# Kernel optimization log

Measured on AMD Instinct MI355X. Metric: run time of the kernel, lower is better.

Reference implementation:

```python
import jax, jax.numpy as jnp
import numpy as np

B, G = 256, 24
N = B * G
D_IN, HEADS, D_HEAD = 128, 8, 64  # out_channels = in_channels//2 = 64, concat=False
EFF = HEADS * D_HEAD
EPS = 1e-5
SCALE = float(np.sqrt(D_HEAD))

def _gelu(x):
    return jax.nn.gelu(x, approximate=False)

def _pff(x, w1, b1, w2, b2):
    # PositionwiseFeedForward, dropout=0 (eval)
    return _gelu(x @ w1.T + b1) @ w2.T + b2

def _graph_norm_global(x, w, b, ms):
    # GraphNorm called without batch -> single graph over all N nodes
    mean = jnp.mean(x, axis=0, keepdims=True)
    out = x - mean * ms
    var = jnp.mean(out * out, axis=0, keepdims=True)
    return w * out / jnp.sqrt(var + EPS) + b

def _graph_norm(x, w, b, ms, batch, nseg):
    cnt = jax.ops.segment_sum(jnp.ones((x.shape[0],), x.dtype), batch, nseg)[:, None]
    mean = jax.ops.segment_sum(x, batch, nseg) / cnt
    out = x - mean[batch] * ms
    var = jax.ops.segment_sum(out * out, batch, nseg) / cnt
    return w * out / jnp.sqrt(var + EPS)[batch] + b

def _segment_softmax(logits, seg, nseg):
    m = jax.ops.segment_max(logits, seg, num_segments=nseg)
    e = jnp.exp(logits - m[seg])
    s = jax.ops.segment_sum(e, seg, num_segments=nseg)
    return e / (s[seg] + 1e-16)

def _attn_conv(x, edge_index, p):
    (nq_w, nq_b, nq_ms, wq, bq, wk, bk, wv, bv,
     no_w, no_b, no_ms, o_w1, o_b1, o_w2, o_b2) = p
    n = x.shape[0]
    xin = x
    xn = _graph_norm_global(x, nq_w, nq_b, nq_ms)
    q = (xn @ wq.T + bq).reshape(n, HEADS, D_HEAD)
    k = (xn @ wk.T + bk).reshape(n, HEADS, D_HEAD)
    v = (xn @ wv.T + bv).reshape(n, HEADS, D_HEAD)
    loops = jnp.arange(n, dtype=edge_index.dtype)  # add_self_loops appends
    src = jnp.concatenate([edge_index[0], loops])
    dst = jnp.concatenate([edge_index[1], loops])
    qk = jnp.sum(q[dst] * k[src], axis=-1) / SCALE          # [E', H]
    alpha = _segment_softmax(qk, dst, n)                     # segment softmax over dst
    aggr = jax.ops.segment_sum(v[src] * alpha[:, :, None], dst, num_segments=n)  # [N,H,Dh]
    aggr = aggr.mean(axis=1)                                 # concat=False: head mean -> [N,64]
    init = xin.reshape(n, D_IN // D_HEAD, D_HEAD).sum(axis=1)  # sum-fold 128 -> 64 residual
    h = aggr + init
    hn = _graph_norm_global(h, no_w, no_b, no_ms)
    return h + _pff(hn, o_w1, o_b1, o_w2, o_b2)


def setup_inputs() -> dict:
    key = jax.random.key(0)
    ks = jax.random.split(key, 12)
    # block-dense edges: fully connected within each set, no self loops
    a = np.arange(G)
    ii, jj = np.meshgrid(a, a, indexing='ij')
    m = ii != jj
    dst_l, src_l = ii[m], jj[m]
    offs = (np.arange(B) * G)[:, None]
    src = (src_l[None, :] + offs).reshape(-1)
    dst = (dst_l[None, :] + offs).reshape(-1)
    edge_index = jnp.asarray(np.stack([src, dst]), dtype=jnp.int64)
    batch = jnp.asarray(np.repeat(np.arange(B), G), dtype=jnp.int64)
    ptr = jnp.asarray(np.arange(B + 1) * G, dtype=jnp.int64)
    x = jax.random.normal(ks[0], (N, D_IN), jnp.float32)
    def lin(k, o, i):
        return jax.random.normal(k, (o, i), jnp.float32) * (1.0 / np.sqrt(i))
    d = dict(x=x, edge_index=edge_index, ptr=ptr, batch=batch)
    d.update(nq_w=jnp.ones((D_IN,)), nq_b=jnp.zeros((D_IN,)), nq_ms=jnp.ones((D_IN,)))
    d.update(wq=lin(ks[1], EFF, D_IN), bq=jnp.zeros((EFF,)),
             wk=lin(ks[2], EFF, D_IN), bk=jnp.zeros((EFF,)),
             wv=lin(ks[3], EFF, D_IN), bv=jnp.zeros((EFF,)))
    d.update(no_w=jnp.ones((D_HEAD,)), no_b=jnp.zeros((D_HEAD,)), no_ms=jnp.ones((D_HEAD,)))
    d.update(o_w1=lin(ks[4], D_HEAD, D_HEAD), o_b1=jnp.zeros((D_HEAD,)),
             o_w2=lin(ks[5], D_HEAD, D_HEAD), o_b2=jnp.zeros((D_HEAD,)))
    d.update(pn_w=jnp.ones((D_HEAD,)), pn_b=jnp.zeros((D_HEAD,)), pn_ms=jnp.ones((D_HEAD,)))
    d.update(p_w1=lin(ks[6], D_HEAD, D_HEAD), p_b1=jnp.zeros((D_HEAD,)),
             p_w2=lin(ks[7], 1, D_HEAD), p_b2=jnp.zeros((1,)))
    return d


def reference(x, edge_index, ptr, batch,
              nq_w, nq_b, nq_ms, wq, bq, wk, bk, wv, bv,
              no_w, no_b, no_ms, o_w1, o_b1, o_w2, o_b2,
              pn_w, pn_b, pn_ms, p_w1, p_b1, p_w2, p_b2):
    nseg = ptr.shape[0] - 1
    h = _attn_conv(x, edge_index,
                   (nq_w, nq_b, nq_ms, wq, bq, wk, bk, wv, bv,
                    no_w, no_b, no_ms, o_w1, o_b1, o_w2, o_b2))   # [N,64]
    hn = _graph_norm(h, pn_w, pn_b, pn_ms, batch, nseg)
    score = _pff(hn, p_w1, p_b1, p_w2, p_b2)                       # [N,1]
    w = _segment_softmax(score[:, 0], batch, nseg)[:, None]        # per-set softmax
    return jax.ops.segment_sum(x * w, batch, num_segments=nseg)    # [B, 128]
```

## Files before the change

### kernel.cpp

```cpp
#include <hip/hip_runtime.h>
#include <stdint.h>


#define N_NODES 6144
#define GSIZE 24
#define NGRAPH 256
#define DIN 128
#define DH 64
#define EFF 512
#define EPSN 1e-5f

typedef __attribute__((ext_vector_type(8))) __bf16 bf16x8;
typedef __attribute__((ext_vector_type(4))) float f32x4;
union U16B { uint4 u; bf16x8 v; unsigned short s[8]; };

__device__ inline unsigned short f2bf(float f){
  unsigned u = __float_as_uint(f);
  u += 0x7fff + ((u>>16)&1);
  return (unsigned short)(u>>16);
}
__device__ inline float gelu_exact(float x){ return 0.5f*x*(1.0f+erff(x*0.70710678118654752f)); }

#define XS    0
#define HS    256
#define WT1   81920
#define WT2   86016
#define PWT1  90112
#define FBo   94208
#define WCVT_BYTE  385024
#define HCOMB_BYTE 778240

#define QSTRIDE 516

__global__ __launch_bounds__(256)
void k_pre(const float* __restrict__ x,
           const float* __restrict__ o_w1, const float* __restrict__ o_w2,
           const float* __restrict__ p_w1,
           const float* __restrict__ o_b1, const float* __restrict__ o_b2,
           const float* __restrict__ p_b1, const float* __restrict__ p_w2,
           const float* __restrict__ p_b2,
           const float* __restrict__ wq, const float* __restrict__ wk,
           const float* __restrict__ wv,
           float* __restrict__ wsf){
  int t = threadIdx.x;
  int bi = blockIdx.x;
  if(bi < 192){
    int c = t & 127, h = t >> 7;
    float s = 0.f, q = 0.f;
    #pragma unroll
    for(int r = 0; r < 16; ++r){
      float v = x[(size_t)(bi*32 + h + 2*r)*DIN + c];
      s += v; q += v*v;
    }
    __shared__ float sm[256], sm2[256];
    sm[t] = s; sm2[t] = q;
    __syncthreads();
    if(t < 128){
      atomicAdd(&wsf[XS + t],       sm[t] + sm[t+128]);
      atomicAdd(&wsf[XS + 128 + t], sm2[t] + sm2[t+128]);
    }
    return;
  }
  if(bi < 195){
    const float* src; float* dst;
    if(bi == 192){ src = o_w1; dst = wsf + WT1; }
    else if(bi == 193){ src = o_w2; dst = wsf + WT2; }
    else { src = p_w1; dst = wsf + PWT1; }
    for(int p = t; p < DH*DH; p += 256){
      int r = p >> 6, c = p & 63;
      dst[c*DH + r] = src[p];
    }
    if(bi == 192){
      float* fb = wsf + FBo;
      if(t < 64){
        fb[t]       = o_b1[t];
        fb[64 + t]  = o_b2[t];
        fb[128 + t] = p_b1[t];
        fb[192 + t] = p_w2[t];
      }
      if(t == 0) fb[256] = p_b2[0];
    }
    return;
  }
  int j = bi - 195;
  int mat = j >> 2, seg = j & 3;
  const float* src = (mat==0) ? wq : (mat==1) ? wk : wv;
  unsigned short* dst = (unsigned short*)((char*)wsf + WCVT_BYTE)
                        + (size_t)mat*EFF*DIN + seg*16384;
  const float* sp = src + seg*16384;
  for(int e = t*8; e < 16384; e += 2048){
    float4 a = *(const float4*)(sp + e);
    float4 b = *(const float4*)(sp + e + 4);
    U16B o;
    o.s[0]=f2bf(a.x); o.s[1]=f2bf(a.y); o.s[2]=f2bf(a.z); o.s[3]=f2bf(a.w);
    o.s[4]=f2bf(b.x); o.s[5]=f2bf(b.y); o.s[6]=f2bf(b.z); o.s[7]=f2bf(b.w);
    *(uint4*)(dst + e) = o.u;
  }
}

#define LOADW(nt, W, B) do{ \
  const int mat_ = (nt)>>2, sub_ = (nt)&3; \
  const unsigned short* wp_ = wcvt + (size_t)mat_*EFF*DIN \
      + (size_t)(h*64 + sub_*16 + m)*DIN + lq*8; \
  W[0] = *(const uint4*)(wp_);      W[1] = *(const uint4*)(wp_ + 32); \
  W[2] = *(const uint4*)(wp_ + 64); W[3] = *(const uint4*)(wp_ + 96); \
  const float* bias_ = (mat_==0) ? bq : (mat_==1) ? bk : bv; \
  B = *(const float4*)(bias_ + h*64 + sub_*16 + lq*4); \
}while(0)

#define COMPW(nt, W, B) do{ \
  const int mat_ = (nt)>>2, sub_ = (nt)&3; \
  f32x4 a0_ = {0.f,0.f,0.f,0.f}, a1_ = {0.f,0.f,0.f,0.f}; \
  U16B w8_; \
  w8_.u = W[0]; \
  a0_ = __builtin_amdgcn_mfma_f32_16x16x32_bf16(w8_.v, afr[0][0], a0_, 0, 0, 0); \
  a1_ = __builtin_amdgcn_mfma_f32_16x16x32_bf16(w8_.v, afr[1][0], a1_, 0, 0, 0); \
  w8_.u = W[1]; \
  a0_ = __builtin_amdgcn_mfma_f32_16x16x32_bf16(w8_.v, afr[0][1], a0_, 0, 0, 0); \
  a1_ = __builtin_amdgcn_mfma_f32_16x16x32_bf16(w8_.v, afr[1][1], a1_, 0, 0, 0); \
  w8_.u = W[2]; \
  a0_ = __builtin_amdgcn_mfma_f32_16x16x32_bf16(w8_.v, afr[0][2], a0_, 0, 0, 0); \
  a1_ = __builtin_amdgcn_mfma_f32_16x16x32_bf16(w8_.v, afr[1][2], a1_, 0, 0, 0); \
  w8_.u = W[3]; \
  a0_ = __builtin_amdgcn_mfma_f32_16x16x32_bf16(w8_.v, afr[0][3], a0_, 0, 0, 0); \
  a1_ = __builtin_amdgcn_mfma_f32_16x16x32_bf16(w8_.v, afr[1][3], a1_, 0, 0, 0); \
  float* dst_ = qlds + mat_*(GSIZE*QSTRIDE); \
  const int col_ = h*64 + sub_*16 + lq*4; \
  { float4 o_; o_.x=a0_[0]+B.x; o_.y=a0_[1]+B.y; o_.z=a0_[2]+B.z; o_.w=a0_[3]+B.w; \
    *(float4*)(dst_ + m*QSTRIDE + col_) = o_; } \
  if(m < 8){ float4 o_; o_.x=a1_[0]+B.x; o_.y=a1_[1]+B.y; o_.z=a1_[2]+B.z; o_.w=a1_[3]+B.w; \
    *(float4*)(dst_ + (16+m)*QSTRIDE + col_) = o_; } \
}while(0)

__global__ __launch_bounds__(512)
void k_attn2(const float* __restrict__ x,
             const float* __restrict__ bq, const float* __restrict__ bk,
             const float* __restrict__ bv,
             const float* __restrict__ nq_w, const float* __restrict__ nq_b,
             const float* __restrict__ nq_ms,
             float* __restrict__ ws, float* __restrict__ hcomb){
  __shared__ __align__(16) float qlds[3*GSIZE*QSTRIDE];
  __shared__ __align__(16) float hv[GSIZE][68];
  __shared__ float A1s[DIN], C1s[DIN];

  int t = threadIdx.x, g = blockIdx.x, base = g*GSIZE;
  int h = t >> 6, l = t & 63;
  const unsigned short* wcvt = (const unsigned short*)((const char*)ws + WCVT_BYTE);

  for(int i = t; i < GSIZE*68; i += 512) ((float*)hv)[i] = 0.f;

  if(t < 128){
    float s1 = ws[XS + t];
    float q1 = ws[XS + 128 + t];
    float mean = s1 * (1.0f / N_NODES);
    float ex2  = q1 * (1.0f / N_NODES);
    float cm   = mean * nq_ms[t];
    float var  = ex2 - 2.f*cm*mean + cm*cm;
    float rstd = rsqrtf(var + EPSN);
    float a    = nq_w[t] * rstd;
    A1s[t] = a; C1s[t] = nq_b[t] - a*cm;
  }
  __syncthreads();

  int m = l & 15, lq = l >> 4;

  bf16x8 afr[2][4];
  #pragma unroll
  for(int mt = 0; mt < 2; ++mt){
    int row = mt*16 + m; if(row > GSIZE-1) row = GSIZE-1;
    const float* xr = x + (size_t)(base + row)*DIN;
    #pragma unroll
    for(int kk = 0; kk < 4; ++kk){
      int k0 = kk*32 + lq*8;
      float4 a = *(const float4*)(xr + k0);
      float4 b = *(const float4*)(xr + k0 + 4);
      U16B u;
      u.s[0] = f2bf(a.x*A1s[k0+0] + C1s[k0+0]);
      u.s[1] = f2bf(a.y*A1s[k0+1] + C1s[k0+1]);
      u.s[2] = f2bf(a.z*A1s[k0+2] + C1s[k0+2]);
      u.s[3] = f2bf(a.w*A1s[k0+3] + C1s[k0+3]);
      u.s[4] = f2bf(b.x*A1s[k0+4] + C1s[k0+4]);
      u.s[5] = f2bf(b.y*A1s[k0+5] + C1s[k0+5]);
      u.s[6] = f2bf(b.z*A1s[k0+6] + C1s[k0+6]);
      u.s[7] = f2bf(b.w*A1s[k0+7] + C1s[k0+7]);
      afr[mt][kk] = u.v;
    }
  }

  {
    uint4 wA[4], wB[4], wC[4];
    float4 bA, bB, bC;
    LOADW(0, wA, bA);  LOADW(1, wB, bB);
    LOADW(2, wC, bC);  COMPW(0, wA, bA);
    LOADW(3, wA, bA);  COMPW(1, wB, bB);
    LOADW(4, wB, bB);  COMPW(2, wC, bC);
    LOADW(5, wC, bC);  COMPW(3, wA, bA);
    LOADW(6, wA, bA);  COMPW(4, wB, bB);
    LOADW(7, wB, bB);  COMPW(5, wC, bC);
    LOADW(8, wC, bC);  COMPW(6, wA, bA);
    LOADW(9, wA, bA);  COMPW(7, wB, bB);
    LOADW(10, wB, bB); COMPW(8, wC, bC);
    LOADW(11, wC, bC); COMPW(9, wA, bA);
    COMPW(10, wB, bB);
    COMPW(11, wC, bC);
  }

  {
    int r0 = 3*(l >> 3), j0 = 3*(l & 7);
    const float* qp = qlds + r0*QSTRIDE + h*64;
    const float* kp = qlds + GSIZE*QSTRIDE + j0*QSTRIDE + h*64;
    float s00=0.f,s01=0.f,s02=0.f,s10=0.f,s11=0.f,s12=0.f,s20=0.f,s21=0.f,s22=0.f;
    #pragma unroll
    for(int d4 = 0; d4 < 16; ++d4){
      float4 q0 = *(const float4*)(qp + d4*4);
      float4 q1 = *(const float4*)(qp + QSTRIDE + d4*4);
      float4 q2 = *(const float4*)(qp + 2*QSTRIDE + d4*4);
      float4 k0 = *(const float4*)(kp + d4*4);
      float4 k1 = *(const float4*)(kp + QSTRIDE + d4*4);
      float4 k2 = *(const float4*)(kp + 2*QSTRIDE + d4*4);
      s00 += q0.x*k0.x + q0.y*k0.y + q0.z*k0.z + q0.w*k0.w;
      s01 += q0.x*k1.x + q0.y*k1.y + q0.z*k1.z + q0.w*k1.w;
      s02 += q0.x*k2.x + q0.y*k2.y + q0.z*k2.z + q0.w*k2.w;
      s10 += q1.x*k0.x + q1.y*k0.y + q1.z*k0.z + q1.w*k0.w;
      s11 += q1.x*k1.x + q1.y*k1.y + q1.z*k1.z + q1.w*k1.w;
      s12 += q1.x*k2.x + q1.y*k2.y + q1.z*k2.z + q1.w*k2.w;
      s20 += q2.x*k0.x + q2.y*k0.y + q2.z*k0.z + q2.w*k0.w;
      s21 += q2.x*k1.x + q2.y*k1.y + q2.z*k1.z + q2.w*k1.w;
      s22 += q2.x*k2.x + q2.y*k2.y + q2.z*k2.z + q2.w*k2.w;
    }
    float a0, a1, a2, m0, su, inv;
    float* STb = qlds + h*64;
    a0 = s00*0.125f; a1 = s01*0.125f; a2 = s02*0.125f;
    m0 = fmaxf(fmaxf(a0, a1), a2);
    #pragma unroll
    for(int o = 1; o < 8; o <<= 1) m0 = fmaxf(m0, __shfl_xor(m0, o, 8));
    a0 = __expf(a0-m0); a1 = __expf(a1-m0); a2 = __expf(a2-m0);
    su = a0 + a1 + a2;
    #pragma unroll
    for(int o = 1; o < 8; o <<= 1) su += __shfl_xor(su, o, 8);
    inv = 1.0f/(su + 1e-16f);
    STb[(j0+0)*QSTRIDE + r0] = a0*inv; STb[(j0+1)*QSTRIDE + r0] = a1*inv; STb[(j0+2)*QSTRIDE + r0] = a2*inv;
    a0 = s10*0.125f; a1 = s11*0.125f; a2 = s12*0.125f;
    m0 = fmaxf(fmaxf(a0, a1), a2);
    #pragma unroll
    for(int o = 1; o < 8; o <<= 1) m0 = fmaxf(m0, __shfl_xor(m0, o, 8));
    a0 = __expf(a0-m0); a1 = __expf(a1-m0); a2 = __expf(a2-m0);
    su = a0 + a1 + a2;
    #pragma unroll
    for(int o = 1; o < 8; o <<= 1) su += __shfl_xor(su, o, 8);
    inv = 1.0f/(su + 1e-16f);
    STb[(j0+0)*QSTRIDE + r0+1] = a0*inv; STb[(j0+1)*QSTRIDE + r0+1] = a1*inv; STb[(j0+2)*QSTRIDE + r0+1] = a2*inv;
    a0 = s20*0.125f; a1 = s21*0.125f; a2 = s22*0.125f;
    m0 = fmaxf(fmaxf(a0, a1), a2);
    #pragma unroll
    for(int o = 1; o < 8; o <<= 1) m0 = fmaxf(m0, __shfl_xor(m0, o, 8));
    a0 = __expf(a0-m0); a1 = __expf(a1-m0); a2 = __expf(a2-m0);
    su = a0 + a1 + a2;
    #pragma unroll
    for(int o = 1; o < 8; o <<= 1) su += __shfl_xor(su, o, 8);
    inv = 1.0f/(su + 1e-16f);
    STb[(j0+0)*QSTRIDE + r0+2] = a0*inv; STb[(j0+1)*QSTRIDE + r0+2] = a1*inv; STb[(j0+2)*QSTRIDE + r0+2] = a2*inv;
  }

  {
    float o24[GSIZE];
    #pragma unroll
    for(int r = 0; r < GSIZE; ++r) o24[r] = 0.f;
    const float* vp  = qlds + 2*GSIZE*QSTRIDE + h*64 + l;
    const float* STb = qlds + h*64;
    #pragma unroll
    for(int j = 0; j < GSIZE; ++j){
      float v = vp[j*QSTRIDE];
      #pragma unroll
      for(int rq = 0; rq < 6; ++rq){
        float4 p4 = *(const float4*)(STb + j*QSTRIDE + rq*4);
        o24[rq*4+0] = fmaf(p4.x, v, o24[rq*4+0]);
        o24[rq*4+1] = fmaf(p4.y, v, o24[rq*4+1]);
        o24[rq*4+2] = fmaf(p4.z, v, o24[rq*4+2]);
        o24[rq*4+3] = fmaf(p4.w, v, o24[rq*4+3]);
      }
    }
    #pragma unroll
    for(int r = 0; r < GSIZE; ++r) atomicAdd(&hv[r][l], o24[r]);
  }
  __syncthreads();

  #pragma unroll
  for(int sl = 0; sl < 3; ++sl){
    int idx = t + sl*512;
    int r = idx >> 6, d = idx & 63;
    const float* xr = x + (size_t)(base + r)*DIN;
    float hval = hv[r][d]*0.125f + xr[d] + xr[64 + d];
    hcomb[(size_t)(base + r)*DH + d] = hval;
    hv[r][d] = hval;
  }
  __syncthreads();
  if(t < 64){
    float s1 = 0.f, s2 = 0.f;
    #pragma unroll
    for(int i = 0; i < GSIZE; ++i){ float v = hv[i][t]; s1 += v; s2 += v*v; }
    atomicAdd(&ws[HS + t],      s1);
    atomicAdd(&ws[HS + 64 + t], s2);
  }
}

__global__ __launch_bounds__(256)
void k_final(const float* __restrict__ x,
             const float* __restrict__ hbuf, const float* __restrict__ ws,
             const float* __restrict__ no_w, const float* __restrict__ no_b,
             const float* __restrict__ no_ms,
             const float* __restrict__ pn_w, const float* __restrict__ pn_b,
             const float* __restrict__ pn_ms,
             float* __restrict__ out){
  __shared__ __align__(16) float W1[4096];
  __shared__ __align__(16) float W2[4096];
  __shared__ __align__(16) float PW1[4096];
  __shared__ __align__(16) float fbs[260];
  __shared__ __align__(16) float hs[GSIZE][68];
  __shared__ __align__(16) float hn[GSIZE][68];
  __shared__ __align__(16) float ts[GSIZE][68];
  __shared__ float A2s[DH], C2s[DH];
  __shared__ float a3[DH], c3[DH];
  __shared__ float scores[GSIZE], wsm[GSIZE];

  int t = threadIdx.x;
  int base = blockIdx.x * GSIZE;
  int c = t & 63, i0 = t >> 6;

  {
    const float4* s1 = (const float4*)(ws + WT1);
    const float4* s2 = (const float4*)(ws + WT2);
    const float4* s3 = (const float4*)(ws + PWT1);
    #pragma unroll
    for(int it = 0; it < 4; ++it){
      int i = t + it*256;
      ((float4*)W1)[i]  = s1[i];
      ((float4*)W2)[i]  = s2[i];
      ((float4*)PW1)[i] = s3[i];
    }
    if(t < 257) fbs[t] = ws[FBo + t];
    if(t < DH){
      float a1 = ws[HS + t];
      float a2 = ws[HS + 64 + t];
      float mean = a1 * (1.0f / N_NODES);
      float ex2  = a2 * (1.0f / N_NODES);
      float cm   = mean * no_ms[t];
      float var  = ex2 - 2.f*cm*mean + cm*cm;
      float rstd = rsqrtf(var + EPSN);
      float a    = no_w[t] * rstd;
      A2s[t] = a; C2s[t] = no_b[t] - a*cm;
    }
  }
  __syncthreads();
  {
    float a2 = A2s[c];
    float c2 = C2s[c];
    #pragma unroll
    for(int r = 0; r < 6; ++r){
      int i = i0 + 4*r;
      float hvv = hbuf[(size_t)(base + i)*DH + c];
      hs[i][c] = hvv;
      hn[i][c] = a2*hvv + c2;
    }
  }
  __syncthreads();

  {
    float acc[6];
    #pragma unroll
    for(int r = 0; r < 6; ++r) acc[r] = fbs[c];
    #pragma unroll 16
    for(int k = 0; k < DH; ++k){
      float w = W1[k*DH + c];
      #pragma unroll
      for(int r = 0; r < 6; ++r) acc[r] = fmaf(hn[i0 + 4*r][k], w, acc[r]);
    }
    #pragma unroll
    for(int r = 0; r < 6; ++r) ts[i0 + 4*r][c] = gelu_exact(acc[r]);
  }
  __syncthreads();

  {
    float acc[6];
    #pragma unroll
    for(int r = 0; r < 6; ++r) acc[r] = fbs[64 + c];
    #pragma unroll 16
    for(int k = 0; k < DH; ++k){
      float w = W2[k*DH + c];
      #pragma unroll
      for(int r = 0; r < 6; ++r) acc[r] = fmaf(ts[i0 + 4*r][k], w, acc[r]);
    }
    #pragma unroll
    for(int r = 0; r < 6; ++r) hs[i0 + 4*r][c] += acc[r];
  }
  __syncthreads();

  if(t < DH){
    float s1 = 0.f, s2 = 0.f;
    #pragma unroll
    for(int i = 0; i < GSIZE; i++){ float v = hs[i][t]; s1 += v; s2 += v*v; }
    float mean = s1 * (1.0f / GSIZE);
    float ex2  = s2 * (1.0f / GSIZE);
    float cm   = mean * pn_ms[t];
    float var  = ex2 - 2.f*cm*mean + cm*cm;
    float rstd = rsqrtf(var + EPSN);
    float a    = pn_w[t] * rstd;
    a3[t] = a; c3[t] = pn_b[t] - a*cm;
  }
  __syncthreads();

  {
    float acc[6];
    #pragma unroll
    for(int r = 0; r < 6; ++r) acc[r] = fbs[128 + c];
    #pragma unroll 16
    for(int k = 0; k < DH; ++k){
      float w  = PW1[k*DH + c];
      float ak = a3[k], ck = c3[k];
      #pragma unroll
      for(int r = 0; r < 6; ++r){
        float hnv = fmaf(ak, hs[i0 + 4*r][k], ck);
        acc[r] = fmaf(hnv, w, acc[r]);
      }
    }
    #pragma unroll
    for(int r = 0; r < 6; ++r) ts[i0 + 4*r][c] = gelu_exact(acc[r]);
  }
  __syncthreads();

  if(t < GSIZE){
    const float4* tp = (const float4*)ts[t];
    const float4* wp = (const float4*)(fbs + 192);
    float s = fbs[256];
    #pragma unroll
    for(int q = 0; q < 16; ++q){
      float4 a = tp[q], b = wp[q];
      s += a.x*b.x + a.y*b.y + a.z*b.z + a.w*b.w;
    }
    scores[t] = s;
  }
  __syncthreads();
  if(t < GSIZE){
    float mx = -1e30f;
    #pragma unroll
    for(int j = 0; j < GSIZE; j++) mx = fmaxf(mx, scores[j]);
    float sum = 0.f;
    #pragma unroll
    for(int j = 0; j < GSIZE; j++) sum += __expf(scores[j] - mx);
    wsm[t] = __expf(scores[t] - mx) / (sum + 1e-16f);
  }
  __syncthreads();
  if(t < DIN){
    float s = 0.f;
    #pragma unroll 8
    for(int i = 0; i < GSIZE; i++) s += wsm[i] * x[(size_t)(base+i)*DIN + t];
    out[(size_t)blockIdx.x*DIN + t] = s;
  }
}

extern "C" void kernel_launch(void* const* d_in, const int* in_sizes, int n_in,
                              void* d_out, int out_size, void* d_ws, size_t ws_size,
                              hipStream_t stream){
  (void)in_sizes; (void)n_in; (void)out_size; (void)ws_size;
  const float* x    = (const float*)d_in[0];
  const float* nq_w = (const float*)d_in[4];
  const float* nq_b = (const float*)d_in[5];
  const float* nq_ms= (const float*)d_in[6];
  const float* wq   = (const float*)d_in[7];
  const float* bq   = (const float*)d_in[8];
  const float* wk   = (const float*)d_in[9];
  const float* bk   = (const float*)d_in[10];
  const float* wv   = (const float*)d_in[11];
  const float* bv   = (const float*)d_in[12];
  const float* no_w = (const float*)d_in[13];
  const float* no_b = (const float*)d_in[14];
  const float* no_ms= (const float*)d_in[15];
  const float* o_w1 = (const float*)d_in[16];
  const float* o_b1 = (const float*)d_in[17];
  const float* o_w2 = (const float*)d_in[18];
  const float* o_b2 = (const float*)d_in[19];
  const float* pn_w = (const float*)d_in[20];
  const float* pn_b = (const float*)d_in[21];
  const float* pn_ms= (const float*)d_in[22];
  const float* p_w1 = (const float*)d_in[23];
  const float* p_b1 = (const float*)d_in[24];
  const float* p_w2 = (const float*)d_in[25];
  const float* p_b2 = (const float*)d_in[26];

  float* ws    = (float*)d_ws;
  float* hcomb = (float*)((char*)d_ws + HCOMB_BYTE);

  hipMemsetAsync(d_ws, 0, 384*sizeof(float), stream);
  k_pre<<<207, 256, 0, stream>>>(x, o_w1, o_w2, p_w1, o_b1, o_b2, p_b1, p_w2, p_b2,
                                 wq, wk, wv, ws);
  k_attn2<<<NGRAPH, 512, 0, stream>>>(x, bq, bk, bv, nq_w, nq_b, nq_ms, ws, hcomb);
  k_final<<<NGRAPH, 256, 0, stream>>>(x, hcomb, ws, no_w, no_b, no_ms,
                                      pn_w, pn_b, pn_ms, (float*)d_out);
}
```

Before: 171.2 us.

## Double k_attn2 block to 1024 threads, splitting projection, scores and PV across halves

Launches the attention kernel with 1024 threads per graph instead of 512. Two wave groups per head split the work: each half computes six of the twelve Q/K/V projection tiles, score dot products are split over the head dimension and combined with a shuffle, and the PV accumulation is split over source nodes. This targets the long serial per-thread chains with only 256 blocks on the GPU. The cost is extra block-wide barriers and higher register pressure under the 1024-thread launch bound.

After: 191.3 us. 1.12x slower.

```diff
diff --git a/kernel.cpp b/kernel.cpp
--- a/kernel.cpp
+++ b/kernel.cpp
@@ -132,7 +132,7 @@
     *(float4*)(dst_ + (16+m)*QSTRIDE + col_) = o_; } \
 }while(0)
 
-__global__ __launch_bounds__(512)
+__global__ __launch_bounds__(1024)
 void k_attn2(const float* __restrict__ x,
              const float* __restrict__ bq, const float* __restrict__ bk,
              const float* __restrict__ bv,
@@ -144,10 +144,11 @@
   __shared__ float A1s[DIN], C1s[DIN];
 
   int t = threadIdx.x, g = blockIdx.x, base = g*GSIZE;
-  int h = t >> 6, l = t & 63;
+  int w = t >> 6, l = t & 63;
+  int h = w & 7, half = w >> 3;
   const unsigned short* wcvt = (const unsigned short*)((const char*)ws + WCVT_BYTE);
 
-  for(int i = t; i < GSIZE*68; i += 512) ((float*)hv)[i] = 0.f;
+  for(int i = t; i < GSIZE*68; i += 1024) ((float*)hv)[i] = 0.f;
 
   if(t < 128){
     float s1 = ws[XS + t];
@@ -190,28 +191,25 @@
   {
     uint4 wA[4], wB[4], wC[4];
     float4 bA, bB, bC;
-    LOADW(0, wA, bA);  LOADW(1, wB, bB);
-    LOADW(2, wC, bC);  COMPW(0, wA, bA);
-    LOADW(3, wA, bA);  COMPW(1, wB, bB);
-    LOADW(4, wB, bB);  COMPW(2, wC, bC);
-    LOADW(5, wC, bC);  COMPW(3, wA, bA);
-    LOADW(6, wA, bA);  COMPW(4, wB, bB);
-    LOADW(7, wB, bB);  COMPW(5, wC, bC);
-    LOADW(8, wC, bC);  COMPW(6, wA, bA);
-    LOADW(9, wA, bA);  COMPW(7, wB, bB);
-    LOADW(10, wB, bB); COMPW(8, wC, bC);
-    LOADW(11, wC, bC); COMPW(9, wA, bA);
-    COMPW(10, wB, bB);
-    COMPW(11, wC, bC);
-  }
-
-  {
-    int r0 = 3*(l >> 3), j0 = 3*(l & 7);
-    const float* qp = qlds + r0*QSTRIDE + h*64;
-    const float* kp = qlds + GSIZE*QSTRIDE + j0*QSTRIDE + h*64;
-    float s00=0.f,s01=0.f,s02=0.f,s10=0.f,s11=0.f,s12=0.f,s20=0.f,s21=0.f,s22=0.f;
-    #pragma unroll
-    for(int d4 = 0; d4 < 16; ++d4){
+    int nb = half*6;
+    LOADW(nb+0, wA, bA);  LOADW(nb+1, wB, bB);
+    LOADW(nb+2, wC, bC);  COMPW(nb+0, wA, bA);
+    LOADW(nb+3, wA, bA);  COMPW(nb+1, wB, bB);
+    LOADW(nb+4, wB, bB);  COMPW(nb+2, wC, bC);
+    LOADW(nb+5, wC, bC);  COMPW(nb+3, wA, bA);
+    COMPW(nb+4, wB, bB);
+    COMPW(nb+5, wC, bC);
+  }
+  __syncthreads();
+
+  int r0 = half*12 + 3*(l >> 4), j0 = 3*(l & 7);
+  float s00=0.f,s01=0.f,s02=0.f,s10=0.f,s11=0.f,s12=0.f,s20=0.f,s21=0.f,s22=0.f;
+  {
+    int d8 = (l >> 3) & 1;
+    const float* qp = qlds + r0*QSTRIDE + h*64 + d8*32;
+    const float* kp = qlds + GSIZE*QSTRIDE + j0*QSTRIDE + h*64 + d8*32;
+    #pragma unroll
+    for(int d4 = 0; d4 < 8; ++d4){
       float4 q0 = *(const float4*)(qp + d4*4);
       float4 q1 = *(const float4*)(qp + QSTRIDE + d4*4);
       float4 q2 = *(const float4*)(qp + 2*QSTRIDE + d4*4);
@@ -228,6 +226,13 @@
       s21 += q2.x*k1.x + q2.y*k1.y + q2.z*k1.z + q2.w*k1.w;
       s22 += q2.x*k2.x + q2.y*k2.y + q2.z*k2.z + q2.w*k2.w;
     }
+    s00 += __shfl_xor(s00, 8); s01 += __shfl_xor(s01, 8); s02 += __shfl_xor(s02, 8);
+    s10 += __shfl_xor(s10, 8); s11 += __shfl_xor(s11, 8); s12 += __shfl_xor(s12, 8);
+    s20 += __shfl_xor(s20, 8); s21 += __shfl_xor(s21, 8); s22 += __shfl_xor(s22, 8);
+  }
+  __syncthreads();
+
+  {
     float a0, a1, a2, m0, su, inv;
     float* STb = qlds + h*64;
     a0 = s00*0.125f; a1 = s01*0.125f; a2 = s02*0.125f;
@@ -261,6 +266,7 @@
     inv = 1.0f/(su + 1e-16f);
     STb[(j0+0)*QSTRIDE + r0+2] = a0*inv; STb[(j0+1)*QSTRIDE + r0+2] = a1*inv; STb[(j0+2)*QSTRIDE + r0+2] = a2*inv;
   }
+  __syncthreads();
 
   {
     float o24[GSIZE];
@@ -268,8 +274,10 @@
     for(int r = 0; r < GSIZE; ++r) o24[r] = 0.f;
     const float* vp  = qlds + 2*GSIZE*QSTRIDE + h*64 + l;
     const float* STb = qlds + h*64;
-    #pragma unroll
-    for(int j = 0; j < GSIZE; ++j){
+    int jb = half*12;
+    #pragma unroll
+    for(int jj = 0; jj < 12; ++jj){
+      int j = jb + jj;
       float v = vp[j*QSTRIDE];
       #pragma unroll
       for(int rq = 0; rq < 6; ++rq){
@@ -286,13 +294,15 @@
   __syncthreads();
 
   #pragma unroll
-  for(int sl = 0; sl < 3; ++sl){
-    int idx = t + sl*512;
-    int r = idx >> 6, d = idx & 63;
-    const float* xr = x + (size_t)(base + r)*DIN;
-    float hval = hv[r][d]*0.125f + xr[d] + xr[64 + d];
-    hcomb[(size_t)(base + r)*DH + d] = hval;
-    hv[r][d] = hval;
+  for(int sl = 0; sl < 2; ++sl){
+    int idx = t + sl*1024;
+    if(idx < GSIZE*64){
+      int r = idx >> 6, d = idx & 63;
+      const float* xr = x + (size_t)(base + r)*DIN;
+      float hval = hv[r][d]*0.125f + xr[d] + xr[64 + d];
+      hcomb[(size_t)(base + r)*DH + d] = hval;
+      hv[r][d] = hval;
+    }
   }
   __syncthreads();
   if(t < 64){
@@ -493,7 +503,7 @@
   hipMemsetAsync(d_ws, 0, 384*sizeof(float), stream);
   k_pre<<<207, 256, 0, stream>>>(x, o_w1, o_w2, p_w1, o_b1, o_b2, p_b1, p_w2, p_b2,
                                  wq, wk, wv, ws);
-  k_attn2<<<NGRAPH, 512, 0, stream>>>(x, bq, bk, bv, nq_w, nq_b, nq_ms, ws, hcomb);
+  k_attn2<<<NGRAPH, 1024, 0, stream>>>(x, bq, bk, bv, nq_w, nq_b, nq_ms, ws, hcomb);
   k_final<<<NGRAPH, 256, 0, stream>>>(x, hcomb, ws, no_w, no_b, no_ms,
                                       pn_w, pn_b, pn_ms, (float*)d_out);
 }
```
